# Kernel tuning notes

Measured on AMD Instinct MI355X. Metric: run time of the kernel, lower is better.

Reference implementation:

```python
import jax, jax.numpy as jnp
import numpy as np


def setup_inputs() -> dict:
    key = jax.random.key(0)
    k0, k1 = jax.random.split(key)
    b, n, m, e = 8, 2048, 2048, 1024
    mat_0 = jax.random.normal(k0, (b, n, e), dtype=jnp.float32)
    mat_1 = jax.random.normal(k1, (b, m, e), dtype=jnp.float32)
    return {"mat_0": mat_0, "mat_1": mat_1}


def reference(mat_0, mat_1):
    # Original tiles to [b,n,m,e], multiplies, and sums over e.
    # Mathematically identical to a batched QK^T matmul: [b,n,m].
    return jnp.einsum('bne,bme->bnm', mat_0, mat_1)
```

## Files before the change

kernel.cpp:

```cpp
#include <hip/hip_runtime.h>
#include <hip/hip_bf16.h>

typedef __attribute__((ext_vector_type(8))) short short8;
typedef __attribute__((ext_vector_type(4))) float f32x4;
typedef __attribute__((ext_vector_type(4))) unsigned int u32x4;
typedef unsigned short u16;

static constexpr int BATCH = 8;
static constexpr int NDIM  = 2048;
static constexpr int MDIM  = 2048;
static constexpr int EDIM  = 1024;
static constexpr int BM    = 128;
static constexpr int BN    = 128;
static constexpr int BK    = 32;
static constexpr int KIT   = EDIM / BK;
static constexpr int LSTR  = 40;

__device__ __forceinline__ unsigned pk(float lo, float hi) {
  return __builtin_amdgcn_perm(__float_as_uint(hi), __float_as_uint(lo), 0x07060302u);
}
__device__ __forceinline__ u32x4 pack8(f32x4 x, f32x4 y) {
  u32x4 r;
  r[0] = pk(x[0], x[1]); r[1] = pk(x[2], x[3]);
  r[2] = pk(y[0], y[1]); r[3] = pk(y[2], y[3]);
  return r;
}

__global__ __launch_bounds__(256, 3)
void bmm_bt_kernel(const float* __restrict__ A, const float* __restrict__ B,
                   float* __restrict__ C) {
  __shared__ u16 As[BM * LSTR];
  __shared__ u16 Bs[BN * LSTR];

  const int tid  = threadIdx.x;
  const int lane = tid & 63;
  const int wave = tid >> 6;
  const int quad = lane >> 4;
  const int ml   = lane & 15;
  const int wrow = (wave >> 1) * 64;
  const int wcol = (wave & 1) * 64;

  const int tcol  = blockIdx.x;
  const int trow  = blockIdx.y;
  const int batch = blockIdx.z;

  const float* Ab = A + (size_t)batch * NDIM * EDIM + (size_t)trow * BM * EDIM;
  const float* Bb = B + (size_t)batch * MDIM * EDIM + (size_t)tcol * BN * EDIM;
  float*       Cb = C + (size_t)batch * NDIM * MDIM;

  const int r0 = tid >> 2;
  const int p0 = (tid & 3) * 8;
  const int r1 = r0 + 64;

  const float* pA0 = Ab + (size_t)r0 * EDIM + p0;
  const float* pA1 = Ab + (size_t)r1 * EDIM + p0;
  const float* pB0 = Bb + (size_t)r0 * EDIM + p0;
  const float* pB1 = Bb + (size_t)r1 * EDIM + p0;

  u16* wA0 = &As[r0 * LSTR + p0];
  u16* wA1 = &As[r1 * LSTR + p0];
  u16* wB0 = &Bs[r0 * LSTR + p0];
  u16* wB1 = &Bs[r1 * LSTR + p0];

  f32x4 a0 = *(const f32x4*)(pA0);
  f32x4 a1 = *(const f32x4*)(pA0 + 4);
  f32x4 a2 = *(const f32x4*)(pA1);
  f32x4 a3 = *(const f32x4*)(pA1 + 4);
  f32x4 b0 = *(const f32x4*)(pB0);
  f32x4 b1 = *(const f32x4*)(pB0 + 4);
  f32x4 b2 = *(const f32x4*)(pB1);
  f32x4 b3 = *(const f32x4*)(pB1 + 4);

  f32x4 acc[4][4] = {};

  for (int kb = 0; kb < KIT; ++kb) {
    __syncthreads();
    *(u32x4*)wA0 = pack8(a0, a1);
    *(u32x4*)wA1 = pack8(a2, a3);
    *(u32x4*)wB0 = pack8(b0, b1);
    *(u32x4*)wB1 = pack8(b2, b3);
    __syncthreads();

    if (kb + 1 < KIT) {
      const int off = (kb + 1) * BK;
      a0 = *(const f32x4*)(pA0 + off);
      a1 = *(const f32x4*)(pA0 + off + 4);
      a2 = *(const f32x4*)(pA1 + off);
      a3 = *(const f32x4*)(pA1 + off + 4);
      b0 = *(const f32x4*)(pB0 + off);
      b1 = *(const f32x4*)(pB0 + off + 4);
      b2 = *(const f32x4*)(pB1 + off);
      b3 = *(const f32x4*)(pB1 + off + 4);
    }

    short8 af[4], bfr[4];
#pragma unroll
    for (int i = 0; i < 4; ++i)
      af[i] = *(const short8*)&As[(wrow + i * 16 + ml) * LSTR + quad * 8];
#pragma unroll
    for (int i = 0; i < 4; ++i)
      bfr[i] = *(const short8*)&Bs[(wcol + i * 16 + ml) * LSTR + quad * 8];

#pragma unroll
    for (int mi = 0; mi < 4; ++mi)
#pragma unroll
      for (int ni = 0; ni < 4; ++ni)
        acc[mi][ni] = __builtin_amdgcn_mfma_f32_16x16x32_bf16(
            af[mi], bfr[ni], acc[mi][ni], 0, 0, 0);
  }

  const int crow = trow * BM + wrow + quad * 4;
  const int ccol = tcol * BN + wcol + ml;
#pragma unroll
  for (int mi = 0; mi < 4; ++mi) {
#pragma unroll
    for (int ni = 0; ni < 4; ++ni) {
      float* cp = Cb + (size_t)(crow + mi * 16) * MDIM + (ccol + ni * 16);
#pragma unroll
      for (int r = 0; r < 4; ++r)
        cp[(size_t)r * MDIM] = acc[mi][ni][r];
    }
  }
}

extern "C" void kernel_launch(void* const* d_in, const int* in_sizes, int n_in,
                              void* d_out, int out_size, void* d_ws, size_t ws_size,
                              hipStream_t stream) {
  const float* A = (const float*)d_in[0];
  const float* B = (const float*)d_in[1];
  float*       C = (float*)d_out;
  dim3 grid(MDIM / BN, NDIM / BM, BATCH);
  bmm_bt_kernel<<<grid, dim3(256), 0, stream>>>(A, B, C);
}
```

Baseline: 324.5 us.

## Pre-convert inputs to bf16 in workspace and load tiles via async global-to-LDS copies

Adds a separate pass that converts both fp32 inputs to bf16 with round-to-nearest-even and writes them into the workspace. The matmul kernel then streams bf16 tiles straight into LDS using global_load_lds, which halves the bytes read per tile and removes the in-loop fp32 packing. The cost is an extra kernel that reads and writes the full inputs, plus a loop with no register prefetch and an unpadded LDS layout that may cause bank conflicts. The old kernel remains as a fallback when the workspace is too small.

```diff
diff --git a/kernel.cpp b/kernel.cpp
--- a/kernel.cpp
+++ b/kernel.cpp
@@ -5,6 +5,8 @@
 typedef __attribute__((ext_vector_type(4))) float f32x4;
 typedef __attribute__((ext_vector_type(4))) unsigned int u32x4;
 typedef unsigned short u16;
+typedef __attribute__((address_space(1))) void gvoid;
+typedef __attribute__((address_space(3))) void lvoid;
 
 static constexpr int BATCH = 8;
 static constexpr int NDIM  = 2048;
@@ -14,7 +16,115 @@
 static constexpr int BN    = 128;
 static constexpr int BK    = 32;
 static constexpr int KIT   = EDIM / BK;
-static constexpr int LSTR  = 40;
+
+__device__ __forceinline__ unsigned bf16rne_pair(float a, float b) {
+  unsigned ua = __float_as_uint(a), ub = __float_as_uint(b);
+  ua = (ua + 0x7FFFu + ((ua >> 16) & 1u)) >> 16;
+  ub = (ub + 0x7FFFu + ((ub >> 16) & 1u)) >> 16;
+  return ua | (ub << 16);
+}
+
+__global__ __launch_bounds__(256)
+void cvt_kernel(const float* __restrict__ A, const float* __restrict__ B,
+                u16* __restrict__ Abf, u16* __restrict__ Bbf) {
+  const int half = (BATCH * NDIM * EDIM) / (256 * 8);
+  int bid = blockIdx.x;
+  const float* src; u16* dst;
+  if (bid < half) { src = A; dst = Abf; }
+  else            { src = B; dst = Bbf; bid -= half; }
+  size_t idx = ((size_t)bid * 256 + threadIdx.x) * 8;
+  f32x4 x = *(const f32x4*)(src + idx);
+  f32x4 y = *(const f32x4*)(src + idx + 4);
+  u32x4 r;
+  r[0] = bf16rne_pair(x[0], x[1]);
+  r[1] = bf16rne_pair(x[2], x[3]);
+  r[2] = bf16rne_pair(y[0], y[1]);
+  r[3] = bf16rne_pair(y[2], y[3]);
+  *(u32x4*)(dst + idx) = r;
+}
+
+__device__ __forceinline__ void async_cp16(const void* g, void* l) {
+  __builtin_amdgcn_global_load_lds((gvoid*)g, (lvoid*)l, 16, 0, 0);
+}
+
+__global__ __launch_bounds__(256, 3)
+void bmm_bf16_kernel(const u16* __restrict__ A, const u16* __restrict__ B,
+                     float* __restrict__ C) {
+  __shared__ u16 As[BM * BK];
+  __shared__ u16 Bs[BN * BK];
+
+  const int tid  = threadIdx.x;
+  const int lane = tid & 63;
+  const int wave = tid >> 6;
+  const int quad = lane >> 4;
+  const int ml   = lane & 15;
+  const int wrow = (wave >> 1) * 64;
+  const int wcol = (wave & 1) * 64;
+
+  const int tcol  = blockIdx.x;
+  const int trow  = blockIdx.y;
+  const int batch = blockIdx.z;
+
+  const u16* Ab = A + (size_t)batch * NDIM * EDIM + (size_t)trow * BM * EDIM;
+  const u16* Bb = B + (size_t)batch * MDIM * EDIM + (size_t)tcol * BN * EDIM;
+  float*     Cb = C + (size_t)batch * NDIM * MDIM;
+
+  const int rA0 = wave * 16;
+  const int rA1 = wave * 16 + 64;
+  const int lrow = lane >> 2;
+  const int lcol = (lane & 3) * 8;
+
+  const u16* gA0 = Ab + (size_t)(rA0 + lrow) * EDIM + lcol;
+  const u16* gA1 = Ab + (size_t)(rA1 + lrow) * EDIM + lcol;
+  const u16* gB0 = Bb + (size_t)(rA0 + lrow) * EDIM + lcol;
+  const u16* gB1 = Bb + (size_t)(rA1 + lrow) * EDIM + lcol;
+  u16* lA0 = &As[rA0 * BK];
+  u16* lA1 = &As[rA1 * BK];
+  u16* lB0 = &Bs[rA0 * BK];
+  u16* lB1 = &Bs[rA1 * BK];
+
+  f32x4 acc[4][4] = {};
+
+  for (int kb = 0; kb < KIT; ++kb) {
+    const int ko = kb * BK;
+    __syncthreads();
+    async_cp16(gA0 + ko, lA0);
+    async_cp16(gA1 + ko, lA1);
+    async_cp16(gB0 + ko, lB0);
+    async_cp16(gB1 + ko, lB1);
+    __syncthreads();
+
+    short8 af[4], bfr[4];
+#pragma unroll
+    for (int i = 0; i < 4; ++i)
+      af[i] = *(const short8*)&As[(wrow + i * 16 + ml) * BK + quad * 8];
+#pragma unroll
+    for (int i = 0; i < 4; ++i)
+      bfr[i] = *(const short8*)&Bs[(wcol + i * 16 + ml) * BK + quad * 8];
+
+#pragma unroll
+    for (int mi = 0; mi < 4; ++mi)
+#pragma unroll
+      for (int ni = 0; ni < 4; ++ni)
+        acc[mi][ni] = __builtin_amdgcn_mfma_f32_16x16x32_bf16(
+            af[mi], bfr[ni], acc[mi][ni], 0, 0, 0);
+  }
+
+  const int crow = trow * BM + wrow + quad * 4;
+  const int ccol = tcol * BN + wcol + ml;
+#pragma unroll
+  for (int mi = 0; mi < 4; ++mi) {
+#pragma unroll
+    for (int ni = 0; ni < 4; ++ni) {
+      float* cp = Cb + (size_t)(crow + mi * 16) * MDIM + (ccol + ni * 16);
+#pragma unroll
+      for (int r = 0; r < 4; ++r)
+        cp[(size_t)r * MDIM] = acc[mi][ni][r];
+    }
+  }
+}
+
+static constexpr int LSTR = 40;
 
 __device__ __forceinline__ unsigned pk(float lo, float hi) {
   return __builtin_amdgcn_perm(__float_as_uint(hi), __float_as_uint(lo), 0x07060302u);
@@ -129,6 +239,19 @@
   const float* A = (const float*)d_in[0];
   const float* B = (const float*)d_in[1];
   float*       C = (float*)d_out;
-  dim3 grid(MDIM / BN, NDIM / BM, BATCH);
-  bmm_bt_kernel<<<grid, dim3(256), 0, stream>>>(A, B, C);
-}
+
+  const size_t elems = (size_t)BATCH * NDIM * EDIM;
+  const size_t need  = 2 * elems * sizeof(u16);
+
+  if (ws_size >= need) {
+    u16* Abf = (u16*)d_ws;
+    u16* Bbf = Abf + elems;
+    const int cvt_blocks = (int)(2 * elems / (256 * 8));
+    cvt_kernel<<<cvt_blocks, 256, 0, stream>>>(A, B, Abf, Bbf);
+    dim3 grid(MDIM / BN, NDIM / BM, BATCH);
+    bmm_bf16_kernel<<<grid, dim3(256), 0, stream>>>(Abf, Bbf, C);
+  } else {
+    dim3 grid(MDIM / BN, NDIM / BM, BATCH);
+    bmm_bt_kernel<<<grid, dim3(256), 0, stream>>>(A, B, C);
+  }
+}
```

Measured after the change: 301.6 us. -7.0%, faster.
